# Optimization experiments

Measured on AMD Instinct MI355X. Metric: run time of the kernel, lower is better.

The kernel has to match this reference:

```python
import jax, jax.numpy as jnp
import numpy as np

D_MODEL = 1024
D_STATE = 16
D_CONV = 4
EXPAND = 2
DT_RANK = 64
D_INNER = EXPAND * D_MODEL
B, L = 1, 2048


def setup_inputs() -> dict:
    key = jax.random.key(0)
    ks = jax.random.split(key, 10)
    x = jax.random.normal(ks[0], (B, L, D_MODEL), dtype=jnp.float32)
    # linear weights (stored as [out, in], like torch)
    W_in = jax.random.normal(ks[1], (2 * D_INNER, D_MODEL), dtype=jnp.float32) * (1.0 / np.sqrt(D_MODEL))
    conv_w = jax.random.normal(ks[2], (D_INNER, 1, D_CONV), dtype=jnp.float32) * (1.0 / np.sqrt(D_CONV))
    conv_b = jax.random.normal(ks[3], (D_INNER,), dtype=jnp.float32) * 0.02
    W_x = jax.random.normal(ks[4], (DT_RANK + 2 * D_STATE, D_INNER), dtype=jnp.float32) * (1.0 / np.sqrt(D_INNER))
    W_dt = jax.random.normal(ks[5], (D_INNER, DT_RANK), dtype=jnp.float32) * (1.0 / np.sqrt(DT_RANK))
    # dt bias init: inverse-softplus of dt ~ LogUniform(1e-3, 0.1)
    dt = jnp.exp(jax.random.uniform(ks[6], (D_INNER,)) * (np.log(0.1) - np.log(0.001)) + np.log(0.001))
    dt = jnp.clip(dt, 1e-4, None)
    b_dt = dt + jnp.log(-jnp.expm1(-dt))
    # A_log init: log(1..d_state) broadcast over d_inner
    A_log = jnp.log(jnp.broadcast_to(jnp.arange(1, D_STATE + 1, dtype=jnp.float32)[None, :], (D_INNER, D_STATE)))
    D_param = jnp.ones((D_INNER,), dtype=jnp.float32)
    W_out = jax.random.normal(ks[7], (D_MODEL, D_INNER), dtype=jnp.float32) * (1.0 / np.sqrt(D_INNER))
    return dict(x=x, W_in=W_in, conv_w=conv_w, conv_b=conv_b, W_x=W_x,
                W_dt=W_dt, b_dt=b_dt, A_log=A_log, D_param=D_param, W_out=W_out)


def _silu(v):
    return v * jax.nn.sigmoid(v)


def _mamba_forward(x, W_in, conv_w, conv_b, W_x, W_dt, b_dt, A_log, D_param, W_out):
    # in_proj: (B, L, 2*d_inner)
    xz = jnp.einsum('bld,ed->ble', x, W_in)
    x_in, z = jnp.split(xz, 2, axis=-1)  # each (B, L, d_inner)

    # depthwise causal conv1d (torch pads d_conv-1 both sides then truncates -> causal left pad)
    xc = jnp.transpose(x_in, (0, 2, 1))  # (B, d_inner, L)
    xc = jax.lax.conv_general_dilated(
        xc, conv_w,
        window_strides=(1,), padding=[(D_CONV - 1, 0)],
        dimension_numbers=('NCH', 'OIH', 'NCH'),
        feature_group_count=D_INNER)
    xc = xc + conv_b[None, :, None]
    x_conv = _silu(jnp.transpose(xc, (0, 2, 1)))  # (B, L, d_inner)

    # selective SSM
    A = -jnp.exp(A_log)  # (d_inner, d_state)
    x_dbl = jnp.einsum('bld,ed->ble', x_conv, W_x)  # (B, L, dt_rank + 2*d_state)
    dt_low, B_ssm, C = jnp.split(x_dbl, [DT_RANK, DT_RANK + D_STATE], axis=-1)
    dt = jax.nn.softplus(jnp.einsum('blr,dr->bld', dt_low, W_dt) + b_dt)  # (B, L, d_inner)

    dA = jnp.exp(jnp.einsum('bld,dn->bldn', dt, A))                        # (B, L, d_inner, d_state)
    dBx = dt[..., None] * B_ssm[:, :, None, :] * x_conv[..., None]          # dB * x, (B, L, d_inner, d_state)

    def step(h, inp):
        dA_t, dBx_t, C_t = inp          # (B, d, n), (B, d, n), (B, n)
        h = dA_t * h + dBx_t
        y_t = jnp.einsum('bdn,bn->bd', h, C_t)
        return h, y_t

    h0 = jnp.zeros((x.shape[0], D_INNER, D_STATE), dtype=x.dtype)
    xs = (jnp.swapaxes(dA, 0, 1), jnp.swapaxes(dBx, 0, 1), jnp.swapaxes(C, 0, 1))
    _, ys = jax.lax.scan(step, h0, xs)   # ys: (L, B, d_inner)
    y = jnp.swapaxes(ys, 0, 1) + x_conv * D_param  # (B, L, d_inner)

    y = y * _silu(z)
    return jnp.einsum('bld,ed->ble', y, W_out)  # (B, L, d_model)


def reference(x, W_in, conv_w, conv_b, W_x, W_dt, b_dt, A_log, D_param, W_out):
    return _mamba_forward(x, W_in, conv_w, conv_b, W_x, W_dt, b_dt, A_log, D_param, W_out)
```

## Files before the change

kernel.cpp:

```cpp
#include <hip/hip_runtime.h>
#include <math.h>

#define LSEQ   2048
#define DMODEL 1024
#define DINNER 2048
#define DSTATE 16
#define DTRANK 64
#define XCOLS  96
#define CL     32
#define NC     (LSEQ/CL)
#define SSTATE (DINNER*DSTATE)

typedef __attribute__((ext_vector_type(8))) short bf16x8;
typedef __attribute__((ext_vector_type(4))) float f32x4;
typedef unsigned short ushort_t;
typedef unsigned int uint_t;

__device__ __forceinline__ float siluf(float v) { return v / (1.f + __expf(-v)); }

__device__ __forceinline__ ushort_t f2bf(float f) {
    uint_t u = __float_as_uint(f);
    u += 0x7FFFu + ((u >> 16) & 1u);
    return (ushort_t)(u >> 16);
}

__global__ __launch_bounds__(256)
void cast_bf16_kernel(const float* __restrict__ in, ushort_t* __restrict__ outp, int n)
{
    int i = (blockIdx.x * 256 + threadIdx.x) * 8;
    if (i >= n) return;
    float4 v0 = *(const float4*)(in + i);
    float4 v1 = *(const float4*)(in + i + 4);
    bf16x8 r;
    r[0] = (short)f2bf(v0.x); r[1] = (short)f2bf(v0.y);
    r[2] = (short)f2bf(v0.z); r[3] = (short)f2bf(v0.w);
    r[4] = (short)f2bf(v1.x); r[5] = (short)f2bf(v1.y);
    r[6] = (short)f2bf(v1.z); r[7] = (short)f2bf(v1.w);
    *(bf16x8*)(outp + i) = r;
}

__global__ __launch_bounds__(256)
void gemm_bf16(const ushort_t* __restrict__ A,
               const ushort_t* __restrict__ B,
               float* __restrict__ C, int M, int N, int K)
{
    __shared__ ushort_t As[128 * 32];
    __shared__ ushort_t Bs[128 * 32];

    const int tid  = threadIdx.x;
    const int wid  = tid >> 6;
    const int lane = tid & 63;
    const int m0 = blockIdx.x * 128;
    const int n0 = blockIdx.y * 128;
    const int wr = (wid >> 1) * 64;
    const int wc = (wid & 1) * 64;
    const int lr = lane & 15;
    const int lk = (lane >> 4) * 8;

    f32x4 acc[4][4];
#pragma unroll
    for (int m = 0; m < 4; m++)
#pragma unroll
        for (int n = 0; n < 4; n++)
            acc[m][n] = (f32x4){0.f, 0.f, 0.f, 0.f};

    for (int k0 = 0; k0 < K; k0 += 32) {
        __syncthreads();
#pragma unroll
        for (int j = 0; j < 2; j++) {
            const int o   = j * 4096 + tid * 16;
            const int row = o >> 6;
            const int kk  = (o & 63) >> 1;
            __builtin_amdgcn_global_load_lds(
                (const __attribute__((address_space(1))) uint_t*)(A + (size_t)(m0 + row) * K + k0 + kk),
                (__attribute__((address_space(3))) uint_t*)((char*)As + o),
                16, 0, 0);
            __builtin_amdgcn_global_load_lds(
                (const __attribute__((address_space(1))) uint_t*)(B + (size_t)(n0 + row) * K + k0 + kk),
                (__attribute__((address_space(3))) uint_t*)((char*)Bs + o),
                16, 0, 0);
        }
        __syncthreads();

        bf16x8 af[4], bfr[4];
#pragma unroll
        for (int m = 0; m < 4; m++)
            af[m] = *(const bf16x8*)&As[(wr + m * 16 + lr) * 32 + lk];
#pragma unroll
        for (int n = 0; n < 4; n++)
            bfr[n] = *(const bf16x8*)&Bs[(wc + n * 16 + lr) * 32 + lk];
#pragma unroll
        for (int m = 0; m < 4; m++)
#pragma unroll
            for (int n = 0; n < 4; n++)
                acc[m][n] = __builtin_amdgcn_mfma_f32_16x16x32_bf16(af[m], bfr[n], acc[m][n], 0, 0, 0);
    }

    const int er = (lane >> 4) * 4;
    const int ec = lane & 15;
#pragma unroll
    for (int m = 0; m < 4; m++) {
        const int grow = m0 + wr + m * 16 + er;
#pragma unroll
        for (int n = 0; n < 4; n++) {
            const int gcol = n0 + wc + n * 16 + ec;
#pragma unroll
            for (int r = 0; r < 4; r++)
                C[(size_t)(grow + r) * N + gcol] = acc[m][n][r];
        }
    }
}

template<int EPI, int SPLITK>
__global__ __launch_bounds__(256)
void gemm64(const float* __restrict__ A, int lda,
            const float* __restrict__ B, int ldb,
            float* C, int ldc,
            const float* __restrict__ bias,
            int M, int N, int K, int KC)
{
    __shared__ float As[16][68];
    __shared__ float Bs[16][68];
    const int tid = threadIdx.x;
    const int m0 = blockIdx.x * 64;
    const int n0 = blockIdx.y * 64;
    const int kbeg = SPLITK ? blockIdx.z * KC : 0;
    const int kend = SPLITK ? min(K, kbeg + KC) : K;
    const int lr = tid >> 2;
    const int lq = (tid & 3) * 4;
    const int tm = tid >> 4;
    const int tn = tid & 15;

    float acc[4][4];
#pragma unroll
    for (int i = 0; i < 4; i++)
#pragma unroll
        for (int j = 0; j < 4; j++) acc[i][j] = 0.f;

    const bool am = (m0 + lr) < M;
    const bool bn = (n0 + lr) < N;
    const float* Arow = A + (size_t)(m0 + lr) * lda;
    const float* Brow = B + (size_t)(n0 + lr) * ldb;

    for (int k0 = kbeg; k0 < kend; k0 += 16) {
        float4 va = am ? *(const float4*)(Arow + k0 + lq) : make_float4(0,0,0,0);
        float4 vb = bn ? *(const float4*)(Brow + k0 + lq) : make_float4(0,0,0,0);
        __syncthreads();
        As[lq+0][lr]=va.x; As[lq+1][lr]=va.y; As[lq+2][lr]=va.z; As[lq+3][lr]=va.w;
        Bs[lq+0][lr]=vb.x; Bs[lq+1][lr]=vb.y; Bs[lq+2][lr]=vb.z; Bs[lq+3][lr]=vb.w;
        __syncthreads();
#pragma unroll
        for (int kk = 0; kk < 16; kk++) {
            float a_[4], b_[4];
#pragma unroll
            for (int i = 0; i < 4; i++) { a_[i] = As[kk][tm*4+i]; b_[i] = Bs[kk][tn*4+i]; }
#pragma unroll
            for (int i = 0; i < 4; i++)
#pragma unroll
                for (int j = 0; j < 4; j++)
                    acc[i][j] = fmaf(a_[i], b_[j], acc[i][j]);
        }
    }

#pragma unroll
    for (int i = 0; i < 4; i++) {
        int m = m0 + tm*4 + i;
        if (m >= M) continue;
#pragma unroll
        for (int j = 0; j < 4; j++) {
            int n = n0 + tn*4 + j;
            if (n >= N) continue;
            float c = acc[i][j];
            if (SPLITK) {
                atomicAdd(&C[(size_t)m * ldc + n], c);
            } else {
                if (EPI == 1) {
                    c += bias[n];
                    c = (c > 20.f) ? c : log1pf(__expf(c));
                }
                C[(size_t)m * ldc + n] = c;
            }
        }
    }
}

__global__ __launch_bounds__(256)
void conv_silu_kernel(const float* __restrict__ xz,
                      const float* __restrict__ conv_w,
                      const float* __restrict__ conv_b,
                      float* __restrict__ xc)
{
    int idx = blockIdx.x * 256 + threadIdx.x;
    if (idx >= LSEQ * DINNER) return;
    int t = idx / DINNER;
    int d = idx - t * DINNER;
    float acc = conv_b[d];
#pragma unroll
    for (int j = 0; j < 4; j++) {
        int tt = t - 3 + j;
        if (tt >= 0) acc = fmaf(conv_w[d*4 + j], xz[(size_t)tt * (2*DINNER) + d], acc);
    }
    xc[idx] = siluf(acc);
}

__global__ __launch_bounds__(256)
void scan_phase1(const float* __restrict__ dtm,
                 const float* __restrict__ xdbl,
                 const float* __restrict__ xc,
                 const float* __restrict__ A_log,
                 float* __restrict__ Aprod, float* __restrict__ hend)
{
    __shared__ float Bs[CL][16];
    const int tid = threadIdx.x;
    const int d = blockIdx.x * 256 + tid;
    const int c = blockIdx.y;
    const int t0 = c * CL;

    {
        int t = tid >> 3, n = (tid * 2) & 15;
        float2 v = *(const float2*)&xdbl[(size_t)(t0 + t) * XCOLS + DTRANK + n];
        Bs[t][n] = v.x; Bs[t][n + 1] = v.y;
    }

    float a[16];
#pragma unroll
    for (int q = 0; q < 4; q++) {
        f32x4 v = *(const f32x4*)&A_log[(size_t)d * DSTATE + q * 4];
#pragma unroll
        for (int j = 0; j < 4; j++) a[q * 4 + j] = -__expf(v[j]);
    }
    float h[16];
#pragma unroll
    for (int n = 0; n < 16; n++) h[n] = 0.f;
    float sdt = 0.f;

    __syncthreads();

    float dtv = dtm[(size_t)t0 * DINNER + d];
    float xv  = xc[(size_t)t0 * DINNER + d];
    for (int tt = 0; tt < CL; tt++) {
        int tn_ = t0 + ((tt + 1 < CL) ? tt + 1 : tt);
        float dtv_n = dtm[(size_t)tn_ * DINNER + d];
        float xv_n  = xc[(size_t)tn_ * DINNER + d];

        f32x4 Bq[4];
#pragma unroll
        for (int q = 0; q < 4; q++) Bq[q] = *(const f32x4*)&Bs[tt][q * 4];
        float dtx = dtv * xv;
        sdt += dtv;
#pragma unroll
        for (int n = 0; n < 16; n++) {
            float e = __expf(dtv * a[n]);
            h[n] = fmaf(e, h[n], dtx * Bq[n >> 2][n & 3]);
        }
        dtv = dtv_n; xv = xv_n;
    }

#pragma unroll
    for (int n = 0; n < 16; n++) {
        const size_t k = (size_t)c * SSTATE + (size_t)n * DINNER + d;
        hend[k]  = h[n];
        Aprod[k] = __expf(a[n] * sdt);
    }
}

__global__ __launch_bounds__(256)
void scan_phase2(const float* __restrict__ Aprod, float* __restrict__ hend)
{
    const int idx = blockIdx.x * 256 + threadIdx.x;
    float carry = 0.f;
#pragma unroll
    for (int c = 0; c < NC; c++) {
        const size_t k = (size_t)c * SSTATE + idx;
        float oh = hend[k];
        float oA = Aprod[k];
        hend[k] = carry;
        carry = fmaf(oA, carry, oh);
    }
}

__global__ __launch_bounds__(256)
void scan_phase3(const float* __restrict__ dtm,
                 const float* __restrict__ xdbl,
                 const float* __restrict__ xc,
                 const float* __restrict__ A_log,
                 const float* __restrict__ Dp,
                 const float* __restrict__ xz,
                 const float* __restrict__ hinit,
                 ushort_t* __restrict__ yb)
{
    __shared__ float Bs[CL][16];
    __shared__ float Cs[CL][16];
    const int tid = threadIdx.x;
    const int d = blockIdx.x * 256 + tid;
    const int c = blockIdx.y;
    const int t0 = c * CL;

    {
        int r = tid & 127;
        int t = r >> 2, n = (r * 4) & 15;
        const float* src = &xdbl[(size_t)(t0 + t) * XCOLS + DTRANK + ((tid < 128) ? 0 : DSTATE) + n];
        float4 v = *(const float4*)src;
        float* dst = (tid < 128) ? &Bs[t][n] : &Cs[t][n];
        dst[0] = v.x; dst[1] = v.y; dst[2] = v.z; dst[3] = v.w;
    }

    float a[16];
#pragma unroll
    for (int q = 0; q < 4; q++) {
        f32x4 v = *(const f32x4*)&A_log[(size_t)d * DSTATE + q * 4];
#pragma unroll
        for (int j = 0; j < 4; j++) a[q * 4 + j] = -__expf(v[j]);
    }
    const float Dv = Dp[d];
    float h[16];
#pragma unroll
    for (int n = 0; n < 16; n++)
        h[n] = hinit[(size_t)c * SSTATE + (size_t)n * DINNER + d];

    __syncthreads();

    float dtv = dtm[(size_t)t0 * DINNER + d];
    float xv  = xc[(size_t)t0 * DINNER + d];
    for (int tt = 0; tt < CL; tt++) {
        const int t = t0 + tt;
        int tn_ = t0 + ((tt + 1 < CL) ? tt + 1 : tt);
        float dtv_n = dtm[(size_t)tn_ * DINNER + d];
        float xv_n  = xc[(size_t)tn_ * DINNER + d];
        float zv    = xz[(size_t)t * (2 * DINNER) + DINNER + d];

        f32x4 Bq[4], Cq[4];
#pragma unroll
        for (int q = 0; q < 4; q++) {
            Bq[q] = *(const f32x4*)&Bs[tt][q * 4];
            Cq[q] = *(const f32x4*)&Cs[tt][q * 4];
        }
        float dtx = dtv * xv;
        float y = 0.f;
#pragma unroll
        for (int n = 0; n < 16; n++) {
            float e = __expf(dtv * a[n]);
            h[n] = fmaf(e, h[n], dtx * Bq[n >> 2][n & 3]);
            y = fmaf(h[n], Cq[n >> 2][n & 3], y);
        }
        yb[(size_t)t * DINNER + d] = f2bf((y + Dv * xv) * siluf(zv));
        dtv = dtv_n; xv = xv_n;
    }
}

extern "C" void kernel_launch(void* const* d_in, const int* in_sizes, int n_in,
                              void* d_out, int out_size, void* d_ws, size_t ws_size,
                              hipStream_t stream)
{
    const float* x      = (const float*)d_in[0];
    const float* W_in   = (const float*)d_in[1];
    const float* conv_w = (const float*)d_in[2];
    const float* conv_b = (const float*)d_in[3];
    const float* W_x    = (const float*)d_in[4];
    const float* W_dt   = (const float*)d_in[5];
    const float* b_dt   = (const float*)d_in[6];
    const float* A_log  = (const float*)d_in[7];
    const float* D_par  = (const float*)d_in[8];
    const float* W_out  = (const float*)d_in[9];
    float* out = (float*)d_out;
    float* ws  = (float*)d_ws;

    float* xz    = ws;
    float* xc    = xz   + (size_t)LSEQ * 2 * DINNER;
    float* xdbl  = xc   + (size_t)LSEQ * DINNER;
    float* dtm   = xdbl + (size_t)LSEQ * XCOLS;
    float* Aprod = dtm  + (size_t)LSEQ * DINNER;
    float* hend  = Aprod + (size_t)NC * SSTATE;
    ushort_t* xb  = (ushort_t*)(hend + (size_t)NC * SSTATE);
    ushort_t* Wib = xb  + (size_t)LSEQ * DMODEL;
    ushort_t* Wob = Wib + (size_t)(2*DINNER) * DMODEL;
    ushort_t* yb  = Wob + (size_t)DMODEL * DINNER;

    hipLaunchKernelGGL(cast_bf16_kernel, dim3((LSEQ*DMODEL/8)/256), dim3(256), 0, stream,
                       x, xb, LSEQ*DMODEL);
    hipLaunchKernelGGL(cast_bf16_kernel, dim3((2*DINNER*DMODEL/8)/256), dim3(256), 0, stream,
                       W_in, Wib, 2*DINNER*DMODEL);
    hipLaunchKernelGGL(cast_bf16_kernel, dim3((DMODEL*DINNER/8)/256), dim3(256), 0, stream,
                       W_out, Wob, DMODEL*DINNER);

    hipLaunchKernelGGL(gemm_bf16, dim3(LSEQ/128, (2*DINNER)/128), dim3(256), 0, stream,
                       xb, Wib, xz, LSEQ, 2*DINNER, DMODEL);

    hipLaunchKernelGGL(conv_silu_kernel, dim3((LSEQ*DINNER)/256), dim3(256), 0, stream,
                       xz, conv_w, conv_b, xc);

    hipMemsetAsync(xdbl, 0, (size_t)LSEQ * XCOLS * sizeof(float), stream);
    hipLaunchKernelGGL((gemm64<0,1>), dim3(LSEQ/64, 2, 8), dim3(256), 0, stream,
                       xc, DINNER, W_x, DINNER, xdbl, XCOLS, (const float*)nullptr,
                       LSEQ, XCOLS, DINNER, 256);

    hipLaunchKernelGGL((gemm64<1,0>), dim3(LSEQ/64, DINNER/64, 1), dim3(256), 0, stream,
                       xdbl, XCOLS, W_dt, DTRANK, dtm, DINNER, b_dt,
                       LSEQ, DINNER, DTRANK, 0);

    hipLaunchKernelGGL(scan_phase1, dim3(DINNER/256, NC), dim3(256), 0, stream,
                       dtm, xdbl, xc, A_log, Aprod, hend);
    hipLaunchKernelGGL(scan_phase2, dim3(SSTATE/256), dim3(256), 0, stream,
                       Aprod, hend);
    hipLaunchKernelGGL(scan_phase3, dim3(DINNER/256, NC), dim3(256), 0, stream,
                       dtm, xdbl, xc, A_log, D_par, xz, hend, yb);

    hipLaunchKernelGGL(gemm_bf16, dim3(LSEQ/128, DMODEL/128), dim3(256), 0, stream,
                       yb, Wob, out, LSEQ, DMODEL, DINNER);
}
```

Baseline: 223.7 us.

## Double-buffer bf16 GEMM LDS tiles, split-K the out-proj, and fuse cast kernels

The bf16 MFMA GEMM now double-buffers its LDS tiles, issuing the next k-tile's global-to-LDS loads before computing on the current one and waiting only on the older loads. The LDS layout changes to k-block-major. The output projection gets a 2-way split-K with atomicAdd into a zeroed output, to fill more CUs (128 blocks become 256). The three separate fp32-to-bf16 cast launches are merged into one kernel. The changes target load latency, low occupancy in the small GEMM, and launch overhead, at the cost of a memset, atomic traffic and order-dependent float summation.

```diff
diff --git a/kernel.cpp b/kernel.cpp
--- a/kernel.cpp
+++ b/kernel.cpp
@@ -25,37 +25,66 @@
 }
 
 __global__ __launch_bounds__(256)
-void cast_bf16_kernel(const float* __restrict__ in, ushort_t* __restrict__ outp, int n)
+void cast3_kernel(const float* __restrict__ s0, ushort_t* __restrict__ d0, int c0,
+                  const float* __restrict__ s1, ushort_t* __restrict__ d1, int c1,
+                  const float* __restrict__ s2, ushort_t* __restrict__ d2, int c2)
 {
     int i = (blockIdx.x * 256 + threadIdx.x) * 8;
-    if (i >= n) return;
-    float4 v0 = *(const float4*)(in + i);
-    float4 v1 = *(const float4*)(in + i + 4);
+    const float* s; ushort_t* d;
+    if (i < c0)           { s = s0 + i;            d = d0 + i; }
+    else if (i < c0 + c1) { s = s1 + (i - c0);     d = d1 + (i - c0); }
+    else if (i < c0 + c1 + c2) { s = s2 + (i - c0 - c1); d = d2 + (i - c0 - c1); }
+    else return;
+    float4 v0 = *(const float4*)s;
+    float4 v1 = *(const float4*)(s + 4);
     bf16x8 r;
     r[0] = (short)f2bf(v0.x); r[1] = (short)f2bf(v0.y);
     r[2] = (short)f2bf(v0.z); r[3] = (short)f2bf(v0.w);
     r[4] = (short)f2bf(v1.x); r[5] = (short)f2bf(v1.y);
     r[6] = (short)f2bf(v1.z); r[7] = (short)f2bf(v1.w);
-    *(bf16x8*)(outp + i) = r;
-}
-
+    *(bf16x8*)d = r;
+}
+
+__device__ __forceinline__ void stage_tile(const ushort_t* __restrict__ A,
+                                           const ushort_t* __restrict__ B,
+                                           ushort_t* As, ushort_t* Bs,
+                                           int m0, int n0, int K, int k0, int tid)
+{
+#pragma unroll
+    for (int j = 0; j < 2; j++) {
+        const int c   = j * 256 + tid;
+        const int row = c & 127;
+        const int kbi = c >> 7;
+        __builtin_amdgcn_global_load_lds(
+            (const __attribute__((address_space(1))) uint_t*)(A + (size_t)(m0 + row) * K + k0 + kbi * 8),
+            (__attribute__((address_space(3))) uint_t*)((char*)As + c * 16), 16, 0, 0);
+        __builtin_amdgcn_global_load_lds(
+            (const __attribute__((address_space(1))) uint_t*)(B + (size_t)(n0 + row) * K + k0 + kbi * 8),
+            (__attribute__((address_space(3))) uint_t*)((char*)Bs + c * 16), 16, 0, 0);
+    }
+}
+
+template<int SPLITK>
 __global__ __launch_bounds__(256)
 void gemm_bf16(const ushort_t* __restrict__ A,
                const ushort_t* __restrict__ B,
                float* __restrict__ C, int M, int N, int K)
 {
-    __shared__ ushort_t As[128 * 32];
-    __shared__ ushort_t Bs[128 * 32];
+    __shared__ ushort_t As[2][4096];
+    __shared__ ushort_t Bs[2][4096];
 
     const int tid  = threadIdx.x;
     const int wid  = tid >> 6;
     const int lane = tid & 63;
     const int m0 = blockIdx.x * 128;
     const int n0 = blockIdx.y * 128;
+    const int kcnt  = (SPLITK > 1) ? (K / SPLITK) : K;
+    const int kbase = (SPLITK > 1) ? blockIdx.z * kcnt : 0;
+    const int NT = kcnt / 32;
     const int wr = (wid >> 1) * 64;
     const int wc = (wid & 1) * 64;
     const int lr = lane & 15;
-    const int lk = (lane >> 4) * 8;
+    const int kb = lane >> 4;
 
     f32x4 acc[4][4];
 #pragma unroll
@@ -64,36 +93,34 @@
         for (int n = 0; n < 4; n++)
             acc[m][n] = (f32x4){0.f, 0.f, 0.f, 0.f};
 
-    for (int k0 = 0; k0 < K; k0 += 32) {
-        __syncthreads();
-#pragma unroll
-        for (int j = 0; j < 2; j++) {
-            const int o   = j * 4096 + tid * 16;
-            const int row = o >> 6;
-            const int kk  = (o & 63) >> 1;
-            __builtin_amdgcn_global_load_lds(
-                (const __attribute__((address_space(1))) uint_t*)(A + (size_t)(m0 + row) * K + k0 + kk),
-                (__attribute__((address_space(3))) uint_t*)((char*)As + o),
-                16, 0, 0);
-            __builtin_amdgcn_global_load_lds(
-                (const __attribute__((address_space(1))) uint_t*)(B + (size_t)(n0 + row) * K + k0 + kk),
-                (__attribute__((address_space(3))) uint_t*)((char*)Bs + o),
-                16, 0, 0);
-        }
-        __syncthreads();
+    stage_tile(A, B, As[0], Bs[0], m0, n0, K, kbase, tid);
+
+    for (int t = 0; t < NT; t++) {
+        const int cur = t & 1;
+        if (t + 1 < NT) {
+            stage_tile(A, B, As[cur ^ 1], Bs[cur ^ 1], m0, n0, K, kbase + (t + 1) * 32, tid);
+            asm volatile("s_waitcnt vmcnt(4)" ::: "memory");
+        } else {
+            asm volatile("s_waitcnt vmcnt(0)" ::: "memory");
+        }
+        __builtin_amdgcn_s_barrier();
+        __builtin_amdgcn_sched_barrier(0);
 
         bf16x8 af[4], bfr[4];
 #pragma unroll
         for (int m = 0; m < 4; m++)
-            af[m] = *(const bf16x8*)&As[(wr + m * 16 + lr) * 32 + lk];
+            af[m] = *(const bf16x8*)&As[cur][kb * 1024 + (wr + m * 16 + lr) * 8];
 #pragma unroll
         for (int n = 0; n < 4; n++)
-            bfr[n] = *(const bf16x8*)&Bs[(wc + n * 16 + lr) * 32 + lk];
+            bfr[n] = *(const bf16x8*)&Bs[cur][kb * 1024 + (wc + n * 16 + lr) * 8];
 #pragma unroll
         for (int m = 0; m < 4; m++)
 #pragma unroll
             for (int n = 0; n < 4; n++)
                 acc[m][n] = __builtin_amdgcn_mfma_f32_16x16x32_bf16(af[m], bfr[n], acc[m][n], 0, 0, 0);
+
+        __builtin_amdgcn_sched_barrier(0);
+        __builtin_amdgcn_s_barrier();
     }
 
     const int er = (lane >> 4) * 4;
@@ -105,8 +132,12 @@
         for (int n = 0; n < 4; n++) {
             const int gcol = n0 + wc + n * 16 + ec;
 #pragma unroll
-            for (int r = 0; r < 4; r++)
-                C[(size_t)(grow + r) * N + gcol] = acc[m][n][r];
+            for (int r = 0; r < 4; r++) {
+                if (SPLITK > 1)
+                    atomicAdd(&C[(size_t)(grow + r) * N + gcol], acc[m][n][r]);
+                else
+                    C[(size_t)(grow + r) * N + gcol] = acc[m][n][r];
+            }
         }
     }
 }
@@ -376,14 +407,13 @@
     ushort_t* Wob = Wib + (size_t)(2*DINNER) * DMODEL;
     ushort_t* yb  = Wob + (size_t)DMODEL * DINNER;
 
-    hipLaunchKernelGGL(cast_bf16_kernel, dim3((LSEQ*DMODEL/8)/256), dim3(256), 0, stream,
-                       x, xb, LSEQ*DMODEL);
-    hipLaunchKernelGGL(cast_bf16_kernel, dim3((2*DINNER*DMODEL/8)/256), dim3(256), 0, stream,
-                       W_in, Wib, 2*DINNER*DMODEL);
-    hipLaunchKernelGGL(cast_bf16_kernel, dim3((DMODEL*DINNER/8)/256), dim3(256), 0, stream,
-                       W_out, Wob, DMODEL*DINNER);
-
-    hipLaunchKernelGGL(gemm_bf16, dim3(LSEQ/128, (2*DINNER)/128), dim3(256), 0, stream,
+    {
+        int c0 = LSEQ * DMODEL, c1 = 2 * DINNER * DMODEL, c2 = DMODEL * DINNER;
+        hipLaunchKernelGGL(cast3_kernel, dim3(((c0 + c1 + c2) / 8) / 256), dim3(256), 0, stream,
+                           x, xb, c0, W_in, Wib, c1, W_out, Wob, c2);
+    }
+
+    hipLaunchKernelGGL((gemm_bf16<1>), dim3(LSEQ/128, (2*DINNER)/128), dim3(256), 0, stream,
                        xb, Wib, xz, LSEQ, 2*DINNER, DMODEL);
 
     hipLaunchKernelGGL(conv_silu_kernel, dim3((LSEQ*DINNER)/256), dim3(256), 0, stream,
@@ -405,6 +435,7 @@
     hipLaunchKernelGGL(scan_phase3, dim3(DINNER/256, NC), dim3(256), 0, stream,
                        dtm, xdbl, xc, A_log, D_par, xz, hend, yb);
 
-    hipLaunchKernelGGL(gemm_bf16, dim3(LSEQ/128, DMODEL/128), dim3(256), 0, stream,
+    hipMemsetAsync(out, 0, (size_t)LSEQ * DMODEL * sizeof(float), stream);
+    hipLaunchKernelGGL((gemm_bf16<2>), dim3(LSEQ/128, DMODEL/128, 2), dim3(256), 0, stream,
                        yb, Wob, out, LSEQ, DMODEL, DINNER);
 }
```

After: 227.6 us. About the same (+1.7%).
